# Optimization experiments

Measured on AMD Instinct MI355X. Metric: run time of the kernel, lower is better.

The kernel has to match this reference:

```python
import jax, jax.numpy as jnp
import numpy as np

NUM_SLOTS = 128
HIDDEN_DIM = 4096
EMA_ALPHA = 0.1
WRITE_TOP_K = 2048
T_TOKENS = 8192
K_RET = 4
BATCH_IDX = 0


def setup_inputs() -> dict:
    key = jax.random.key(0)
    k1, k2, k3, k4, k5 = jax.random.split(key, 5)
    hidden_states = jax.random.normal(k1, (T_TOKENS, HIDDEN_DIM), dtype=jnp.float32)
    # attention weights over K retrieved slots: normalized to a distribution per token
    raw = jax.random.uniform(k2, (T_TOKENS, K_RET), dtype=jnp.float32)
    attention_weights = raw / raw.sum(axis=-1, keepdims=True)
    slot_indices = jax.random.randint(k3, (T_TOKENS, K_RET), 0, NUM_SLOTS)
    memory = jax.random.normal(k4, (1, NUM_SLOTS, HIDDEN_DIM), dtype=jnp.float32)
    W_imp = jax.random.normal(k5, (1, HIDDEN_DIM), dtype=jnp.float32) * 0.02
    b_imp = jnp.zeros((1,), dtype=jnp.float32)
    return {
        "hidden_states": hidden_states,
        "attention_weights": attention_weights,
        "slot_indices": slot_indices,
        "memory": memory,
        "W_imp": W_imp,
        "b_imp": b_imp,
    }


def _compute_importance(hidden_states, attention_weights, W_imp, b_imp):
    # magnitude: ||h_t||_2, [T]
    magnitude = jnp.linalg.norm(hidden_states, axis=-1)
    # attention surprise: normalized entropy over K slots, [T]
    attn = attention_weights
    entropy = -(attn * jnp.log(attn + 1e-8)).sum(axis=-1)
    max_entropy = jnp.log(jnp.asarray(attn.shape[-1], dtype=jnp.float32))
    surprise = entropy / jnp.maximum(max_entropy, 1e-8)
    importance = magnitude * (1.0 + surprise)  # 'combined' mode
    learned_score = hidden_states @ W_imp[0] + b_imp[0]  # [T]
    return importance + jax.nn.sigmoid(learned_score)


def reference(hidden_states, attention_weights, slot_indices, memory, W_imp, b_imp):
    # importance-based top-K token selection
    importance = _compute_importance(hidden_states, attention_weights, W_imp, b_imp)
    _, topk_idx = jax.lax.top_k(importance, WRITE_TOP_K)
    h_sel = hidden_states[topk_idx]          # [Ksel, D]
    si_sel = slot_indices[topk_idx]          # [Ksel, K]

    # membership[t, n] = 1 if slot n appears anywhere in token t's retrieved slots
    # (matches torch's (slot_indices == idx).any(dim=-1))
    onehot = jax.nn.one_hot(si_sel, NUM_SLOTS, dtype=jnp.float32)  # [Ksel, K, N]
    member = (onehot.sum(axis=1) > 0).astype(jnp.float32)          # [Ksel, N]

    counts = member.sum(axis=0)                                    # [N]
    sums = jnp.einsum("tn,td->nd", member, h_sel)                  # [N, D]
    agg = sums / jnp.maximum(counts, 1.0)[:, None]                 # segment mean

    current = memory[BATCH_IDX]                                    # [N, D]
    updated = EMA_ALPHA * agg + (1.0 - EMA_ALPHA) * current
    new_slots = jnp.where(counts[:, None] > 0, updated, current)
    return memory.at[BATCH_IDX].set(new_slots)
```

## Files before the change

### kernel.cpp

```cpp
#include <hip/hip_runtime.h>
#include <math.h>

#define T_TOK 8192
#define HDIM 4096
#define NSLOT 128
#define KRET 4
#define TOPK 2048
#define ALPHA 0.1f
#define MAXC 2048

__global__ __launch_bounds__(256) void importance_kernel(
    const float* __restrict__ h, const float* __restrict__ attn,
    const float* __restrict__ W, const float* __restrict__ b,
    float* __restrict__ imp, int* __restrict__ rank)
{
    const int wid  = threadIdx.x >> 6;
    const int lane = threadIdx.x & 63;
    const int t = blockIdx.x * 4 + wid;
    const float4* hv = reinterpret_cast<const float4*>(h + (size_t)t * HDIM);
    const float4* Wv = reinterpret_cast<const float4*>(W);
    float sumsq = 0.f, dot = 0.f;
    #pragma unroll 4
    for (int i = 0; i < 16; i++) {
        float4 x = hv[lane + i * 64];
        float4 w = Wv[lane + i * 64];
        sumsq += x.x * x.x + x.y * x.y + x.z * x.z + x.w * x.w;
        dot   += x.x * w.x + x.y * w.y + x.z * w.z + x.w * w.w;
    }
    #pragma unroll
    for (int off = 32; off > 0; off >>= 1) {
        sumsq += __shfl_down(sumsq, off);
        dot   += __shfl_down(dot, off);
    }
    if (lane == 0) {
        float mag = sqrtf(sumsq);
        float ent = 0.f;
        #pragma unroll
        for (int k = 0; k < KRET; k++) {
            float a = attn[t * KRET + k];
            ent -= a * logf(a + 1e-8f);
        }
        float surprise = ent / logf(4.0f);
        float score = dot + b[0];
        float sig = 1.0f / (1.0f + expf(-score));
        imp[t] = mag * (1.0f + surprise) + sig;
        rank[t] = 0;
    }
}

__global__ __launch_bounds__(256) void rank_kernel(
    const float* __restrict__ imp, int* __restrict__ rank)
{
    const int cb = blockIdx.x & 31;
    const int sl = blockIdx.x >> 5;
    __shared__ float tile[256];
    const int base = sl * 256;
    tile[threadIdx.x] = imp[base + threadIdx.x];
    __syncthreads();
    const int t = cb * 256 + threadIdx.x;
    const float mine = imp[t];
    int r = 0;
    #pragma unroll 8
    for (int i = 0; i < 256; i++) {
        float v = tile[i];
        int s = base + i;
        r += (v > mine) || (v == mine && s < t);
    }
    if (r) atomicAdd(&rank[t], r);
}

__global__ __launch_bounds__(256) void slotlist_kernel(
    const int* __restrict__ rank, const int* __restrict__ si,
    int* __restrict__ lists, int* __restrict__ counts)
{
    const int slot = blockIdx.x;
    const int tid = threadIdx.x;
    __shared__ int part[256];
    const int base = tid * 32;
    unsigned mask = 0;
    int local = 0;
    const int4* si4 = reinterpret_cast<const int4*>(si);
    #pragma unroll 8
    for (int j = 0; j < 32; j++) {
        const int t = base + j;
        int4 s = si4[t];
        bool sel = rank[t] < TOPK;
        bool mem = (s.x == slot) | (s.y == slot) | (s.z == slot) | (s.w == slot);
        if (sel && mem) { mask |= (1u << j); local++; }
    }
    part[tid] = local;
    __syncthreads();
    for (int off = 1; off < 256; off <<= 1) {
        int v = part[tid];
        int add = (tid >= off) ? part[tid - off] : 0;
        __syncthreads();
        part[tid] = v + add;
        __syncthreads();
    }
    int pos = part[tid] - local;
    int* mylist = lists + (size_t)slot * MAXC;
    for (int j = 0; j < 32; j++) {
        if (mask & (1u << j)) mylist[pos++] = base + j;
    }
    if (tid == 255) counts[slot] = part[255];
}

__global__ __launch_bounds__(256) void update_kernel(
    const float* __restrict__ h, const float* __restrict__ mem,
    const int* __restrict__ lists, const int* __restrict__ counts,
    float* __restrict__ out)
{
    const int slot = blockIdx.x >> 2;
    const int chunk = blockIdx.x & 3;
    const int cnt = counts[slot];
    __shared__ int s_list[MAXC];
    for (int i = threadIdx.x; i < cnt; i += 256)
        s_list[i] = lists[(size_t)slot * MAXC + i];
    __syncthreads();

    const int dbase = chunk * 1024 + threadIdx.x * 4;
    float4 acc = make_float4(0.f, 0.f, 0.f, 0.f);
    int i = 0;
    for (; i + 4 <= cnt; i += 4) {
        int t0 = s_list[i], t1 = s_list[i + 1];
        int t2 = s_list[i + 2], t3 = s_list[i + 3];
        float4 x0 = *reinterpret_cast<const float4*>(h + (size_t)t0 * HDIM + dbase);
        float4 x1 = *reinterpret_cast<const float4*>(h + (size_t)t1 * HDIM + dbase);
        float4 x2 = *reinterpret_cast<const float4*>(h + (size_t)t2 * HDIM + dbase);
        float4 x3 = *reinterpret_cast<const float4*>(h + (size_t)t3 * HDIM + dbase);
        acc.x += x0.x + x1.x + x2.x + x3.x;
        acc.y += x0.y + x1.y + x2.y + x3.y;
        acc.z += x0.z + x1.z + x2.z + x3.z;
        acc.w += x0.w + x1.w + x2.w + x3.w;
    }
    for (; i < cnt; i++) {
        int t0 = s_list[i];
        float4 x0 = *reinterpret_cast<const float4*>(h + (size_t)t0 * HDIM + dbase);
        acc.x += x0.x; acc.y += x0.y; acc.z += x0.z; acc.w += x0.w;
    }

    const size_t o = (size_t)slot * HDIM + dbase;
    float4 cur = *reinterpret_cast<const float4*>(mem + o);
    float4 r;
    if (cnt > 0) {
        float inv = 1.0f / (float)cnt;
        r.x = ALPHA * (acc.x * inv) + (1.f - ALPHA) * cur.x;
        r.y = ALPHA * (acc.y * inv) + (1.f - ALPHA) * cur.y;
        r.z = ALPHA * (acc.z * inv) + (1.f - ALPHA) * cur.z;
        r.w = ALPHA * (acc.w * inv) + (1.f - ALPHA) * cur.w;
    } else {
        r = cur;
    }
    *reinterpret_cast<float4*>(out + o) = r;
}

extern "C" void kernel_launch(void* const* d_in, const int* in_sizes, int n_in,
                              void* d_out, int out_size, void* d_ws, size_t ws_size,
                              hipStream_t stream) {
    const float* h    = (const float*)d_in[0];
    const float* attn = (const float*)d_in[1];
    const int*   si   = (const int*)d_in[2];
    const float* mem  = (const float*)d_in[3];
    const float* W    = (const float*)d_in[4];
    const float* b    = (const float*)d_in[5];
    float* out = (float*)d_out;

    char* ws = (char*)d_ws;
    float* imp    = (float*)(ws);
    int*   rank   = (int*)(ws + 32768);
    int*   counts = (int*)(ws + 65536);
    int*   lists  = (int*)(ws + 131072);

    importance_kernel<<<T_TOK / 4, 256, 0, stream>>>(h, attn, W, b, imp, rank);
    rank_kernel<<<1024, 256, 0, stream>>>(imp, rank);
    slotlist_kernel<<<NSLOT, 256, 0, stream>>>(rank, si, lists, counts);
    update_kernel<<<NSLOT * 4, 256, 0, stream>>>(h, mem, lists, counts, out);
}
```

Before: 59.90 us.

## Split slot gather-sum across token segments with a separate combine kernel

The per-slot gather-sum is split into four token segments per slot/chunk, giving four times as many blocks. Each segment writes a partial sum to workspace, and a new combine kernel adds the partials and applies the EMA update. This targets low parallelism: 512 blocks each looping over roughly 250 tokens leaves long serial latency chains. The cost is an extra kernel launch plus an 8MB partial write and read, and list indices are now read from global memory instead of shared memory.

```diff
diff --git a/kernel.cpp b/kernel.cpp
--- a/kernel.cpp
+++ b/kernel.cpp
@@ -105,25 +105,24 @@
     if (tid == 255) counts[slot] = part[255];
 }
 
-__global__ __launch_bounds__(256) void update_kernel(
-    const float* __restrict__ h, const float* __restrict__ mem,
-    const int* __restrict__ lists, const int* __restrict__ counts,
-    float* __restrict__ out)
-{
-    const int slot = blockIdx.x >> 2;
-    const int chunk = blockIdx.x & 3;
+__global__ __launch_bounds__(256) void update_partial_kernel(
+    const float* __restrict__ h, const int* __restrict__ lists,
+    const int* __restrict__ counts, float* __restrict__ partial)
+{
+    const int seg   = blockIdx.x & 3;
+    const int chunk = (blockIdx.x >> 2) & 3;
+    const int slot  = blockIdx.x >> 4;
     const int cnt = counts[slot];
-    __shared__ int s_list[MAXC];
-    for (int i = threadIdx.x; i < cnt; i += 256)
-        s_list[i] = lists[(size_t)slot * MAXC + i];
-    __syncthreads();
-
+    const int beg = (cnt * seg) >> 2;
+    const int end = (cnt * (seg + 1)) >> 2;
+    const int* mylist = lists + (size_t)slot * MAXC;
     const int dbase = chunk * 1024 + threadIdx.x * 4;
+
     float4 acc = make_float4(0.f, 0.f, 0.f, 0.f);
-    int i = 0;
-    for (; i + 4 <= cnt; i += 4) {
-        int t0 = s_list[i], t1 = s_list[i + 1];
-        int t2 = s_list[i + 2], t3 = s_list[i + 3];
+    int i = beg;
+    for (; i + 4 <= end; i += 4) {
+        int t0 = mylist[i], t1 = mylist[i + 1];
+        int t2 = mylist[i + 2], t3 = mylist[i + 3];
         float4 x0 = *reinterpret_cast<const float4*>(h + (size_t)t0 * HDIM + dbase);
         float4 x1 = *reinterpret_cast<const float4*>(h + (size_t)t1 * HDIM + dbase);
         float4 x2 = *reinterpret_cast<const float4*>(h + (size_t)t2 * HDIM + dbase);
@@ -133,21 +132,43 @@
         acc.z += x0.z + x1.z + x2.z + x3.z;
         acc.w += x0.w + x1.w + x2.w + x3.w;
     }
-    for (; i < cnt; i++) {
-        int t0 = s_list[i];
+    for (; i < end; i++) {
+        int t0 = mylist[i];
         float4 x0 = *reinterpret_cast<const float4*>(h + (size_t)t0 * HDIM + dbase);
         acc.x += x0.x; acc.y += x0.y; acc.z += x0.z; acc.w += x0.w;
     }
-
+    const size_t o = ((size_t)seg * NSLOT + slot) * HDIM + dbase;
+    *reinterpret_cast<float4*>(partial + o) = acc;
+}
+
+__global__ __launch_bounds__(256) void combine_kernel(
+    const float* __restrict__ partial, const float* __restrict__ mem,
+    const int* __restrict__ counts, float* __restrict__ out)
+{
+    const int slot = blockIdx.x >> 2;
+    const int chunk = blockIdx.x & 3;
+    const int dbase = chunk * 1024 + threadIdx.x * 4;
+    const int cnt = counts[slot];
     const size_t o = (size_t)slot * HDIM + dbase;
+
+    float4 a0 = *reinterpret_cast<const float4*>(partial + ((size_t)0 * NSLOT + slot) * HDIM + dbase);
+    float4 a1 = *reinterpret_cast<const float4*>(partial + ((size_t)1 * NSLOT + slot) * HDIM + dbase);
+    float4 a2 = *reinterpret_cast<const float4*>(partial + ((size_t)2 * NSLOT + slot) * HDIM + dbase);
+    float4 a3 = *reinterpret_cast<const float4*>(partial + ((size_t)3 * NSLOT + slot) * HDIM + dbase);
+    float4 s;
+    s.x = ((a0.x + a1.x) + a2.x) + a3.x;
+    s.y = ((a0.y + a1.y) + a2.y) + a3.y;
+    s.z = ((a0.z + a1.z) + a2.z) + a3.z;
+    s.w = ((a0.w + a1.w) + a2.w) + a3.w;
+
     float4 cur = *reinterpret_cast<const float4*>(mem + o);
     float4 r;
     if (cnt > 0) {
         float inv = 1.0f / (float)cnt;
-        r.x = ALPHA * (acc.x * inv) + (1.f - ALPHA) * cur.x;
-        r.y = ALPHA * (acc.y * inv) + (1.f - ALPHA) * cur.y;
-        r.z = ALPHA * (acc.z * inv) + (1.f - ALPHA) * cur.z;
-        r.w = ALPHA * (acc.w * inv) + (1.f - ALPHA) * cur.w;
+        r.x = ALPHA * (s.x * inv) + (1.f - ALPHA) * cur.x;
+        r.y = ALPHA * (s.y * inv) + (1.f - ALPHA) * cur.y;
+        r.z = ALPHA * (s.z * inv) + (1.f - ALPHA) * cur.z;
+        r.w = ALPHA * (s.w * inv) + (1.f - ALPHA) * cur.w;
     } else {
         r = cur;
     }
@@ -166,13 +187,15 @@
     float* out = (float*)d_out;
 
     char* ws = (char*)d_ws;
-    float* imp    = (float*)(ws);
-    int*   rank   = (int*)(ws + 32768);
-    int*   counts = (int*)(ws + 65536);
-    int*   lists  = (int*)(ws + 131072);
+    float* imp     = (float*)(ws);
+    int*   rank    = (int*)(ws + 32768);
+    int*   counts  = (int*)(ws + 65536);
+    int*   lists   = (int*)(ws + 131072);
+    float* partial = (float*)(ws + 2097152);
 
     importance_kernel<<<T_TOK / 4, 256, 0, stream>>>(h, attn, W, b, imp, rank);
     rank_kernel<<<1024, 256, 0, stream>>>(imp, rank);
     slotlist_kernel<<<NSLOT, 256, 0, stream>>>(rank, si, lists, counts);
-    update_kernel<<<NSLOT * 4, 256, 0, stream>>>(h, mem, lists, counts, out);
-}
+    update_partial_kernel<<<NSLOT * 16, 256, 0, stream>>>(h, lists, counts, partial);
+    combine_kernel<<<NSLOT * 4, 256, 0, stream>>>(partial, mem, counts, out);
+}
```

After: 63.35 us. 5.8% more time.

## Replace pairwise rank top-k with per-block radix select fused into slot listing

Applied to the files above, without the earlier changes.

Removes the O(T^2) pairwise rank kernel and its atomics. Each slot block now loads all importance values into shared memory and runs a 4-pass 8-bit radix select on the float bits to find the top-k threshold, with index-ordered tie breaking. This is then fused with building the slot membership list. It saves a launch and the quadratic compare work, but every one of the 128 blocks repeats the selection redundantly, using 32KB of LDS and many syncthreads. It also depends on importance being non-negative so the raw float bits order correctly.

```diff
diff --git a/kernel.cpp b/kernel.cpp
--- a/kernel.cpp
+++ b/kernel.cpp
@@ -12,7 +12,7 @@
 __global__ __launch_bounds__(256) void importance_kernel(
     const float* __restrict__ h, const float* __restrict__ attn,
     const float* __restrict__ W, const float* __restrict__ b,
-    float* __restrict__ imp, int* __restrict__ rank)
+    float* __restrict__ imp)
 {
     const int wid  = threadIdx.x >> 6;
     const int lane = threadIdx.x & 63;
@@ -44,65 +44,103 @@
         float score = dot + b[0];
         float sig = 1.0f / (1.0f + expf(-score));
         imp[t] = mag * (1.0f + surprise) + sig;
-        rank[t] = 0;
-    }
-}
-
-__global__ __launch_bounds__(256) void rank_kernel(
-    const float* __restrict__ imp, int* __restrict__ rank)
-{
-    const int cb = blockIdx.x & 31;
-    const int sl = blockIdx.x >> 5;
-    __shared__ float tile[256];
-    const int base = sl * 256;
-    tile[threadIdx.x] = imp[base + threadIdx.x];
-    __syncthreads();
-    const int t = cb * 256 + threadIdx.x;
-    const float mine = imp[t];
-    int r = 0;
-    #pragma unroll 8
-    for (int i = 0; i < 256; i++) {
-        float v = tile[i];
-        int s = base + i;
-        r += (v > mine) || (v == mine && s < t);
-    }
-    if (r) atomicAdd(&rank[t], r);
-}
-
-__global__ __launch_bounds__(256) void slotlist_kernel(
-    const int* __restrict__ rank, const int* __restrict__ si,
+    }
+}
+
+__global__ __launch_bounds__(256) void selectlist_kernel(
+    const float* __restrict__ imp, const int* __restrict__ si,
     int* __restrict__ lists, int* __restrict__ counts)
 {
     const int slot = blockIdx.x;
-    const int tid = threadIdx.x;
-    __shared__ int part[256];
+    const int tid  = threadIdx.x;
+    __shared__ unsigned s_u[T_TOK];
+    __shared__ int s_hist[256];
+    __shared__ int s_scan[256];
+    __shared__ unsigned s_prefix;
+    __shared__ int s_want;
+
+    for (int i = tid; i < T_TOK; i += 256)
+        s_u[i] = __float_as_uint(imp[i]);
+    if (tid == 0) { s_prefix = 0u; s_want = TOPK; }
+    __syncthreads();
+
+    for (int pass = 0; pass < 4; pass++) {
+        const int p = 24 - pass * 8;
+        const unsigned himask = (pass == 0) ? 0u : (0xFFFFFFFFu << (p + 8));
+        const unsigned pref = s_prefix;
+        const int want = s_want;
+        s_hist[tid] = 0;
+        __syncthreads();
+        for (int j = tid; j < T_TOK; j += 256) {
+            unsigned u = s_u[j];
+            if ((u & himask) == pref) atomicAdd(&s_hist[(u >> p) & 255], 1);
+        }
+        __syncthreads();
+        s_scan[tid] = s_hist[tid];
+        __syncthreads();
+        for (int off = 1; off < 256; off <<= 1) {
+            int add = (tid + off < 256) ? s_scan[tid + off] : 0;
+            __syncthreads();
+            s_scan[tid] += add;
+            __syncthreads();
+        }
+        int sufb  = s_scan[tid];
+        int sufb1 = (tid < 255) ? s_scan[tid + 1] : 0;
+        if (sufb >= want && sufb1 < want) {
+            s_prefix = pref | ((unsigned)tid << p);
+            s_want = want - sufb1;
+        }
+        __syncthreads();
+    }
+    const unsigned thr = s_prefix;
+    const int ties_allowed = s_want;
+
     const int base = tid * 32;
+    int eqcnt = 0;
+    #pragma unroll 8
+    for (int j = 0; j < 32; j++) eqcnt += (s_u[base + j] == thr);
+    __syncthreads();
+    s_scan[tid] = eqcnt;
+    __syncthreads();
+    for (int off = 1; off < 256; off <<= 1) {
+        int v = s_scan[tid];
+        int add = (tid >= off) ? s_scan[tid - off] : 0;
+        __syncthreads();
+        s_scan[tid] = v + add;
+        __syncthreads();
+    }
+    const int tie_base = s_scan[tid] - eqcnt;
+
+    const int4* si4 = reinterpret_cast<const int4*>(si);
     unsigned mask = 0;
     int local = 0;
-    const int4* si4 = reinterpret_cast<const int4*>(si);
+    int trun = tie_base;
     #pragma unroll 8
     for (int j = 0; j < 32; j++) {
         const int t = base + j;
+        unsigned u = s_u[t];
+        bool sel = (u > thr) || (u == thr && trun < ties_allowed);
+        if (u == thr) trun++;
         int4 s = si4[t];
-        bool sel = rank[t] < TOPK;
         bool mem = (s.x == slot) | (s.y == slot) | (s.z == slot) | (s.w == slot);
         if (sel && mem) { mask |= (1u << j); local++; }
     }
-    part[tid] = local;
+    __syncthreads();
+    s_scan[tid] = local;
     __syncthreads();
     for (int off = 1; off < 256; off <<= 1) {
-        int v = part[tid];
-        int add = (tid >= off) ? part[tid - off] : 0;
-        __syncthreads();
-        part[tid] = v + add;
-        __syncthreads();
-    }
-    int pos = part[tid] - local;
+        int v = s_scan[tid];
+        int add = (tid >= off) ? s_scan[tid - off] : 0;
+        __syncthreads();
+        s_scan[tid] = v + add;
+        __syncthreads();
+    }
+    int pos = s_scan[tid] - local;
     int* mylist = lists + (size_t)slot * MAXC;
     for (int j = 0; j < 32; j++) {
         if (mask & (1u << j)) mylist[pos++] = base + j;
     }
-    if (tid == 255) counts[slot] = part[255];
+    if (tid == 255) counts[slot] = s_scan[255];
 }
 
 __global__ __launch_bounds__(256) void update_kernel(
@@ -167,12 +205,10 @@
 
     char* ws = (char*)d_ws;
     float* imp    = (float*)(ws);
-    int*   rank   = (int*)(ws + 32768);
     int*   counts = (int*)(ws + 65536);
     int*   lists  = (int*)(ws + 131072);
 
-    importance_kernel<<<T_TOK / 4, 256, 0, stream>>>(h, attn, W, b, imp, rank);
-    rank_kernel<<<1024, 256, 0, stream>>>(imp, rank);
-    slotlist_kernel<<<NSLOT, 256, 0, stream>>>(rank, si, lists, counts);
+    importance_kernel<<<T_TOK / 4, 256, 0, stream>>>(h, attn, W, b, imp);
+    selectlist_kernel<<<NSLOT, 256, 0, stream>>>(imp, si, lists, counts);
     update_kernel<<<NSLOT * 4, 256, 0, stream>>>(h, mem, lists, counts, out);
 }
```

After: 64.96 us. 1.08x slower.

## Replace per-slot gather lists with token-segment scatter into shared partial sums

Applied to the files above, without the earlier changes.

The per-slot list build and gather are replaced. Each block takes a segment of tokens and a 64-column chunk of the hidden dimension, compacts the selected tokens with a wave ballot, and scatter-adds each token's values into per-slot accumulators in LDS. A combine kernel then sums the 16 segment partials per slot and applies the EMA. Each selected token row is now read once instead of up to four times, and the serial 128-block list-building kernel goes away. In exchange the code writes and re-reads a 16x128x4096 float partial buffer (about 32 MB) and does scalar 4-byte loads with dependent LDS read-modify-writes.

```diff
diff --git a/kernel.cpp b/kernel.cpp
--- a/kernel.cpp
+++ b/kernel.cpp
@@ -7,7 +7,8 @@
 #define KRET 4
 #define TOPK 2048
 #define ALPHA 0.1f
-#define MAXC 2048
+#define SEGS 16
+#define CHUNKS 64
 
 __global__ __launch_bounds__(256) void importance_kernel(
     const float* __restrict__ h, const float* __restrict__ attn,
@@ -69,74 +70,87 @@
     if (r) atomicAdd(&rank[t], r);
 }
 
-__global__ __launch_bounds__(256) void slotlist_kernel(
-    const int* __restrict__ rank, const int* __restrict__ si,
-    int* __restrict__ lists, int* __restrict__ counts)
+__global__ __launch_bounds__(128) void scatter_kernel(
+    const float* __restrict__ h, const int* __restrict__ rank,
+    const int* __restrict__ si, float* __restrict__ partial,
+    int* __restrict__ pcnt)
 {
-    const int slot = blockIdx.x;
+    const int chunk = blockIdx.x & 63;
+    const int seg   = blockIdx.x >> 6;
     const int tid = threadIdx.x;
-    __shared__ int part[256];
-    const int base = tid * 32;
-    unsigned mask = 0;
-    int local = 0;
+    const int w = tid >> 6, lane = tid & 63;
+
+    __shared__ float s_acc[2][NSLOT * 64];
+    __shared__ int   s_tok[2][256];
+    __shared__ int   s_cnt[2][NSLOT];
+
+    float* acc = s_acc[w];
+    for (int i = tid; i < 2 * NSLOT * 64; i += 128) s_acc[0][i] = 0.f;
+    for (int i = tid; i < 2 * NSLOT; i += 128) s_cnt[0][i] = 0;
+    __syncthreads();
+
+    const int tbase = seg * 512 + w * 256;
+    int n = 0;
+    #pragma unroll
+    for (int it = 0; it < 4; it++) {
+        const int t = tbase + it * 64 + lane;
+        bool sel = rank[t] < TOPK;
+        unsigned long long bal = __ballot(sel);
+        if (sel) {
+            int pos = n + (int)__popcll(bal & ((1ull << lane) - 1ull));
+            s_tok[w][pos] = t;
+        }
+        n += (int)__popcll(bal);
+    }
+
     const int4* si4 = reinterpret_cast<const int4*>(si);
-    #pragma unroll 8
-    for (int j = 0; j < 32; j++) {
-        const int t = base + j;
-        int4 s = si4[t];
-        bool sel = rank[t] < TOPK;
-        bool mem = (s.x == slot) | (s.y == slot) | (s.z == slot) | (s.w == slot);
-        if (sel && mem) { mask |= (1u << j); local++; }
+    const int dbase = chunk * 64 + lane;
+    for (int i = 0; i < n; i++) {
+        const int t = s_tok[w][i];
+        const int4 s4 = si4[t];
+        const float x = h[(size_t)t * HDIM + dbase];
+        bool dy = (s4.y != s4.x);
+        bool dz = (s4.z != s4.x) && (s4.z != s4.y);
+        bool dw = (s4.w != s4.x) && (s4.w != s4.y) && (s4.w != s4.z);
+        acc[s4.x * 64 + lane] += x;
+        if (dy) acc[s4.y * 64 + lane] += x;
+        if (dz) acc[s4.z * 64 + lane] += x;
+        if (dw) acc[s4.w * 64 + lane] += x;
+        if (lane == 0) {
+            s_cnt[w][s4.x]++;
+            if (dy) s_cnt[w][s4.y]++;
+            if (dz) s_cnt[w][s4.z]++;
+            if (dw) s_cnt[w][s4.w]++;
+        }
     }
-    part[tid] = local;
     __syncthreads();
-    for (int off = 1; off < 256; off <<= 1) {
-        int v = part[tid];
-        int add = (tid >= off) ? part[tid - off] : 0;
-        __syncthreads();
-        part[tid] = v + add;
-        __syncthreads();
+
+    for (int i = tid; i < NSLOT * 64; i += 128) {
+        const int slot = i >> 6;
+        const int d = i & 63;
+        partial[((size_t)(seg * NSLOT + slot)) * HDIM + chunk * 64 + d] =
+            s_acc[0][i] + s_acc[1][i];
     }
-    int pos = part[tid] - local;
-    int* mylist = lists + (size_t)slot * MAXC;
-    for (int j = 0; j < 32; j++) {
-        if (mask & (1u << j)) mylist[pos++] = base + j;
-    }
-    if (tid == 255) counts[slot] = part[255];
+    if (chunk == 0 && tid < NSLOT)
+        pcnt[seg * NSLOT + tid] = s_cnt[0][tid] + s_cnt[1][tid];
 }
 
-__global__ __launch_bounds__(256) void update_kernel(
-    const float* __restrict__ h, const float* __restrict__ mem,
-    const int* __restrict__ lists, const int* __restrict__ counts,
-    float* __restrict__ out)
+__global__ __launch_bounds__(256) void combine_kernel(
+    const float* __restrict__ partial, const int* __restrict__ pcnt,
+    const float* __restrict__ mem, float* __restrict__ out)
 {
     const int slot = blockIdx.x >> 2;
-    const int chunk = blockIdx.x & 3;
-    const int cnt = counts[slot];
-    __shared__ int s_list[MAXC];
-    for (int i = threadIdx.x; i < cnt; i += 256)
-        s_list[i] = lists[(size_t)slot * MAXC + i];
-    __syncthreads();
+    const int q = blockIdx.x & 3;
+    const int dbase = q * 1024 + threadIdx.x * 4;
 
-    const int dbase = chunk * 1024 + threadIdx.x * 4;
-    float4 acc = make_float4(0.f, 0.f, 0.f, 0.f);
-    int i = 0;
-    for (; i + 4 <= cnt; i += 4) {
-        int t0 = s_list[i], t1 = s_list[i + 1];
-        int t2 = s_list[i + 2], t3 = s_list[i + 3];
-        float4 x0 = *reinterpret_cast<const float4*>(h + (size_t)t0 * HDIM + dbase);
-        float4 x1 = *reinterpret_cast<const float4*>(h + (size_t)t1 * HDIM + dbase);
-        float4 x2 = *reinterpret_cast<const float4*>(h + (size_t)t2 * HDIM + dbase);
-        float4 x3 = *reinterpret_cast<const float4*>(h + (size_t)t3 * HDIM + dbase);
-        acc.x += x0.x + x1.x + x2.x + x3.x;
-        acc.y += x0.y + x1.y + x2.y + x3.y;
-        acc.z += x0.z + x1.z + x2.z + x3.z;
-        acc.w += x0.w + x1.w + x2.w + x3.w;
-    }
-    for (; i < cnt; i++) {
-        int t0 = s_list[i];
-        float4 x0 = *reinterpret_cast<const float4*>(h + (size_t)t0 * HDIM + dbase);
-        acc.x += x0.x; acc.y += x0.y; acc.z += x0.z; acc.w += x0.w;
+    int cnt = 0;
+    float4 s = make_float4(0.f, 0.f, 0.f, 0.f);
+    #pragma unroll
+    for (int seg = 0; seg < SEGS; seg++) {
+        cnt += pcnt[seg * NSLOT + slot];
+        float4 p = *reinterpret_cast<const float4*>(
+            partial + ((size_t)(seg * NSLOT + slot)) * HDIM + dbase);
+        s.x += p.x; s.y += p.y; s.z += p.z; s.w += p.w;
     }
 
     const size_t o = (size_t)slot * HDIM + dbase;
@@ -144,10 +158,10 @@
     float4 r;
     if (cnt > 0) {
         float inv = 1.0f / (float)cnt;
-        r.x = ALPHA * (acc.x * inv) + (1.f - ALPHA) * cur.x;
-        r.y = ALPHA * (acc.y * inv) + (1.f - ALPHA) * cur.y;
-        r.z = ALPHA * (acc.z * inv) + (1.f - ALPHA) * cur.z;
-        r.w = ALPHA * (acc.w * inv) + (1.f - ALPHA) * cur.w;
+        r.x = ALPHA * (s.x * inv) + (1.f - ALPHA) * cur.x;
+        r.y = ALPHA * (s.y * inv) + (1.f - ALPHA) * cur.y;
+        r.z = ALPHA * (s.z * inv) + (1.f - ALPHA) * cur.z;
+        r.w = ALPHA * (s.w * inv) + (1.f - ALPHA) * cur.w;
     } else {
         r = cur;
     }
@@ -166,13 +180,13 @@
     float* out = (float*)d_out;
 
     char* ws = (char*)d_ws;
-    float* imp    = (float*)(ws);
-    int*   rank   = (int*)(ws + 32768);
-    int*   counts = (int*)(ws + 65536);
-    int*   lists  = (int*)(ws + 131072);
+    float* imp     = (float*)(ws);
+    int*   rank    = (int*)(ws + 32768);
+    int*   pcnt    = (int*)(ws + 65536);
+    float* partial = (float*)(ws + 2097152);
 
     importance_kernel<<<T_TOK / 4, 256, 0, stream>>>(h, attn, W, b, imp, rank);
     rank_kernel<<<1024, 256, 0, stream>>>(imp, rank);
-    slotlist_kernel<<<NSLOT, 256, 0, stream>>>(rank, si, lists, counts);
-    update_kernel<<<NSLOT * 4, 256, 0, stream>>>(h, mem, lists, counts, out);
+    scatter_kernel<<<SEGS * CHUNKS, 128, 0, stream>>>(h, rank, si, partial, pcnt);
+    combine_kernel<<<NSLOT * 4, 256, 0, stream>>>(partial, pcnt, mem, out);
 }
```

New measurement: 163.8 us. +173.4%, slower.
